# Performance work log

Measured on AMD Instinct MI355X. Metric: run time of the kernel, lower is better.

## Reference

```python
import jax, jax.numpy as jnp
import numpy as np

EMB = 1024

def setup_inputs() -> dict:
    key = jax.random.key(0)
    ks = jax.random.split(key, 6)
    B, S, E = 4, 2048, EMB
    x = jax.random.normal(ks[0], (B, S, E), dtype=jnp.float32)
    attention_mask = jax.random.randint(ks[1], (B, S, S), 0, 2, dtype=jnp.int32)
    proj_w = jax.random.normal(ks[2], (E, 3 * E), dtype=jnp.float32) * (1.0 / np.sqrt(E))
    proj_b = jax.random.normal(ks[3], (3 * E,), dtype=jnp.float32) * 0.02
    out_w = jax.random.normal(ks[4], (E, E), dtype=jnp.float32) * (1.0 / np.sqrt(E))
    out_b = jax.random.normal(ks[5], (E,), dtype=jnp.float32) * 0.02
    return {"x": x, "attention_mask": attention_mask, "proj_w": proj_w,
            "proj_b": proj_b, "out_w": out_w, "out_b": out_b}

def reference(x, attention_mask, proj_w, proj_b, out_w, out_b):
    E = x.shape[-1]
    scale = 1.0 / jnp.sqrt(jnp.asarray(E, x.dtype))
    qkv = x @ proj_w + proj_b                      # [B,S,3E]
    q, k, v = jnp.split(qkv, 3, axis=-1)           # each [B,S,E]
    scores = jnp.einsum('bqe,bke->bqk', q, k) * scale  # [B,S,S]
    scores = jnp.where(attention_mask == 0, jnp.asarray(-1e20, scores.dtype), scores)
    attn = jax.nn.softmax(scores, axis=-1)
    ctx = jnp.einsum('bqk,bke->bqe', attn, v)      # [B,S,E]
    return ctx @ out_w + out_b
```

## Files before the change

### kernel.cpp

```cpp
#include <hip/hip_runtime.h>
#include <cstdint>

typedef unsigned short u16;
typedef uint32_t u32;
typedef __bf16 bf16x8 __attribute__((ext_vector_type(8)));
typedef float f32x4 __attribute__((ext_vector_type(4)));

__device__ __forceinline__ u16 f2bf(float f) {
  unsigned u = __float_as_uint(f);
  u += 0x7fffu + ((u >> 16) & 1u);
  return (u16)(u >> 16);
}

__device__ __forceinline__ void async16(const void* g, void* l) {
  __builtin_amdgcn_global_load_lds(
      (const __attribute__((address_space(1))) uint32_t*)g,
      (__attribute__((address_space(3))) uint32_t*)l, 16, 0, 0);
}

__global__ __launch_bounds__(256) void k_prep(const float* __restrict__ x, u16* __restrict__ xb,
                                              const float* __restrict__ pw, u16* __restrict__ wt,
                                              const float* __restrict__ ow, u16* __restrict__ owt,
                                              const int* __restrict__ mask, u32* __restrict__ mbits) {
  const int bid = blockIdx.x;
  if (bid < 8192) {
    const int i = bid * 256 + threadIdx.x;
    const float4 v = ((const float4*)x)[i];
    ushort4 o;
    o.x = f2bf(v.x); o.y = f2bf(v.y); o.z = f2bf(v.z); o.w = f2bf(v.w);
    ((ushort4*)xb)[i] = o;
    return;
  }
  if (bid >= 12288) {
    const size_t w = (size_t)(bid - 12288) * 256 + threadIdx.x;
    const int* p = mask + w * 32;
    u32 bits = 0;
#pragma unroll
    for (int j = 0; j < 8; ++j) {
      const int4 v = ((const int4*)p)[j];
      bits |= (u32)(v.x & 1) << (j * 4 + 0);
      bits |= (u32)(v.y & 1) << (j * 4 + 1);
      bits |= (u32)(v.z & 1) << (j * 4 + 2);
      bits |= (u32)(v.w & 1) << (j * 4 + 3);
    }
    mbits[w] = bits;
    return;
  }
  __shared__ u16 tile[32][33];
  const int tx = threadIdx.x & 31, ty = threadIdx.x >> 5;
  const float* in;
  u16* outp;
  int lda, ldo, c0, r0;
  if (bid < 11264) {
    const int id = bid - 8192;
    c0 = (id % 96) * 32; r0 = (id / 96) * 32;
    in = pw; outp = wt; lda = 3072; ldo = 1024;
  } else {
    const int id = bid - 11264;
    c0 = (id % 32) * 32; r0 = (id / 32) * 32;
    in = ow; outp = owt; lda = 1024; ldo = 1024;
  }
#pragma unroll
  for (int i = 0; i < 4; ++i)
    tile[ty + i * 8][tx] = f2bf(in[(size_t)(r0 + ty + i * 8) * lda + c0 + tx]);
  __syncthreads();
#pragma unroll
  for (int i = 0; i < 4; ++i)
    outp[(size_t)(c0 + ty + i * 8) * ldo + r0 + tx] = tile[tx][ty + i * 8];
}

template <int MODE, int TM>
__global__ __launch_bounds__(256) void gemm_bt(
    const u16* __restrict__ A, long lda, long bsA,
    const u16* __restrict__ Bt, long ldb, long bsB,
    void* __restrict__ C, long ldc, long bsC,
    int M, int N, int K,
    const float* __restrict__ bias, const u32* __restrict__ mbits) {
  constexpr int MT = TM / 32;
  constexpr int ACALLS = TM / 8;
  constexpr int NC = (TM + 128) / 32;
  __shared__ u16 As[TM * 64];
  __shared__ u16 Bs[128 * 64];

  const int b = blockIdx.z;
  const int m0 = blockIdx.y * TM, n0 = blockIdx.x * 128;
  const int lane = threadIdx.x & 63;
  const int w = threadIdx.x >> 6;
  const int wr = w >> 1, wc = w & 1;

  const int srow = lane >> 3;
  const int scol = ((lane & 7) ^ ((lane >> 3) & 7)) * 8;
  const u16* pa = A + (size_t)b * bsA + (size_t)(m0 + srow) * lda + scol;
  const u16* pb = Bt + (size_t)b * bsB + (size_t)(n0 + srow) * ldb + scol;

  const int m_l = lane & 15, q = lane >> 4, m7 = m_l & 7;
  const int offs[2] = {(q ^ m7) * 8, ((4 + q) ^ m7) * 8};

  f32x4 acc[MT][4] = {};
  f32x4 accs[MT] = {};
  bf16x8 ones;
#pragma unroll
  for (int e = 0; e < 8; ++e) ones[e] = (__bf16)1.0f;

  for (int kt = 0; kt < K; kt += 64) {
    __syncthreads();
#pragma unroll
    for (int g = 0; g < NC; ++g) {
      const int idx = w * NC + g;
      if (idx < ACALLS)
        async16(pa + (size_t)(idx * 8) * lda, As + idx * 512);
      else
        async16(pb + (size_t)((idx - ACALLS) * 8) * ldb, Bs + (idx - ACALLS) * 512);
    }
    __syncthreads();
#pragma unroll
    for (int s = 0; s < 2; ++s) {
      bf16x8 af[MT], bfr[4];
#pragma unroll
      for (int t = 0; t < MT; ++t)
        af[t] = *(const bf16x8*)(As + (wr * (TM / 2) + t * 16 + m_l) * 64 + offs[s]);
#pragma unroll
      for (int t = 0; t < 4; ++t)
        bfr[t] = *(const bf16x8*)(Bs + (wc * 64 + t * 16 + m_l) * 64 + offs[s]);
#pragma unroll
      for (int mt = 0; mt < MT; ++mt)
#pragma unroll
        for (int nt = 0; nt < 4; ++nt)
          acc[mt][nt] = __builtin_amdgcn_mfma_f32_16x16x32_bf16(af[mt], bfr[nt], acc[mt][nt], 0, 0, 0);
      if constexpr (MODE == 2) {
#pragma unroll
        for (int mt = 0; mt < MT; ++mt)
          accs[mt] = __builtin_amdgcn_mfma_f32_16x16x32_bf16(af[mt], ones, accs[mt], 0, 0, 0);
      }
    }
    pa += 64;
    pb += 64;
  }

  if constexpr (MODE == 1) {
    __syncthreads();
    const int rl = threadIdx.x >> 1, pr = threadIdx.x & 1;
    const uint2 v = *(const uint2*)(mbits + ((size_t)(b * M + m0 + rl)) * (N >> 5) + (n0 >> 5) + pr * 2);
    ((u32*)As)[rl * 4 + pr * 2] = v.x;
    ((u32*)As)[rl * 4 + pr * 2 + 1] = v.y;
    __syncthreads();
  }

  float rinv[MT][4];
  if constexpr (MODE == 2) {
#pragma unroll
    for (int mt = 0; mt < MT; ++mt)
#pragma unroll
      for (int r = 0; r < 4; ++r) rinv[mt][r] = 1.0f / accs[mt][r];
  }

#pragma unroll
  for (int mt = 0; mt < MT; ++mt) {
#pragma unroll
    for (int nt = 0; nt < 4; ++nt) {
      const int col = n0 + wc * 64 + nt * 16 + m_l;
      const int row0 = m0 + wr * (TM / 2) + mt * 16 + q * 4;
      if constexpr (MODE == 3) {
        ushort4 o;
        o.x = f2bf(acc[mt][nt][0]); o.y = f2bf(acc[mt][nt][1]);
        o.z = f2bf(acc[mt][nt][2]); o.w = f2bf(acc[mt][nt][3]);
        *(ushort4*)((u16*)C + (size_t)b * bsC + (size_t)col * ldc + row0) = o;
      } else {
#pragma unroll
        for (int r = 0; r < 4; ++r) {
          const int row = row0 + r;
          float v = acc[mt][nt][r];
          if constexpr (MODE == 0) {
            v += bias[col];
            if (col < 1024) v *= 0.03125f;
            ((u16*)C)[(size_t)b * bsC + (size_t)row * ldc + col] = f2bf(v);
          } else if constexpr (MODE == 1) {
            const int cl = wc * 64 + nt * 16 + m_l;
            const int rl = wr * 64 + mt * 16 + q * 4 + r;
            const u32 wb = ((const u32*)As)[rl * 4 + (cl >> 5)];
            v = ((wb >> (cl & 31)) & 1u) ? __expf(fminf(v, 30.f)) : 0.f;
            ((u16*)C)[(size_t)b * bsC + (size_t)row * ldc + col] = f2bf(v);
          } else if constexpr (MODE == 2) {
            v = v * rinv[mt][r] + bias[col];
            ((float*)C)[(size_t)b * bsC + (size_t)row * ldc + col] = v;
          }
        }
      }
    }
  }
}

extern "C" void kernel_launch(void* const* d_in, const int* in_sizes, int n_in,
                              void* d_out, int out_size, void* d_ws, size_t ws_size,
                              hipStream_t stream) {
  const float* x = (const float*)d_in[0];
  const int* mask = (const int*)d_in[1];
  const float* proj_w = (const float*)d_in[2];
  const float* proj_b = (const float*)d_in[3];
  const float* out_w = (const float*)d_in[4];
  const float* out_b = (const float*)d_in[5];
  float* out = (float*)d_out;

  char* ws = (char*)d_ws;
  u16* xb = (u16*)(ws);
  u16* wt = (u16*)(ws + 16777216);
  u16* owt = (u16*)(ws + 23068672);
  u16* qkv = (u16*)(ws + 25165824);
  u16* P = (u16*)(ws + 75497472);
  u32* mbits = (u32*)(ws + 109051904);
  u16* Ut = (u16*)xb;

  k_prep<<<14336, 256, 0, stream>>>(x, xb, proj_w, wt, out_w, owt, mask, mbits);
  gemm_bt<0, 128><<<dim3(24, 64, 1), 256, 0, stream>>>(xb, 1024, 0, wt, 1024, 0, qkv, 3072, 0,
                                                       8192, 3072, 1024, proj_b, nullptr);
  gemm_bt<1, 128><<<dim3(16, 16, 4), 256, 0, stream>>>(
      qkv, 3072, (long)2048 * 3072, qkv + 1024, 3072, (long)2048 * 3072,
      P, 2048, (long)2048 * 2048, 2048, 2048, 1024, nullptr, mbits);
  gemm_bt<3, 64><<<dim3(8, 32, 4), 256, 0, stream>>>(
      qkv + 2048, 3072, (long)2048 * 3072, owt, 1024, 0,
      Ut, 2048, (long)1024 * 2048, 2048, 1024, 1024, nullptr, nullptr);
  gemm_bt<2, 64><<<dim3(8, 32, 4), 256, 0, stream>>>(
      P, 2048, (long)2048 * 2048, Ut, 2048, (long)1024 * 2048,
      out, 1024, (long)2048 * 1024, 2048, 1024, 2048, out_b, nullptr);
}
```

Baseline: 342.0 us.

## Merge scores and V-projection GEMMs into one launch, retile final GEMM

Folds the QK^T masked-exp GEMM and the V·Wout^T transpose GEMM, which are independent, into a single kernel that branches on blockIdx.z. The two run concurrently and one launch boundary goes away. The V-projection now uses 128x128 tiles (half the blocks in that z-range exit early). The final P·U GEMM moves to 64x64 tiles for twice as many blocks. The aim is better GPU fill and less launch/tail overhead, at the cost of idle blocks and smaller-tile efficiency in the last GEMM.

New measurement: 379.8 us. 1.11x slower.

```diff
diff --git a/kernel.cpp b/kernel.cpp
--- a/kernel.cpp
+++ b/kernel.cpp
@@ -69,21 +69,18 @@
     outp[(size_t)(c0 + ty + i * 8) * ldo + r0 + tx] = tile[tx][ty + i * 8];
 }
 
-template <int MODE, int TM>
-__global__ __launch_bounds__(256) void gemm_bt(
+template <int MODE, int TM, int BN>
+__device__ __forceinline__ void gemm_core(
+    u16* As, u16* Bs,
     const u16* __restrict__ A, long lda, long bsA,
     const u16* __restrict__ Bt, long ldb, long bsB,
     void* __restrict__ C, long ldc, long bsC,
     int M, int N, int K,
-    const float* __restrict__ bias, const u32* __restrict__ mbits) {
-  constexpr int MT = TM / 32;
-  constexpr int ACALLS = TM / 8;
-  constexpr int NC = (TM + 128) / 32;
-  __shared__ u16 As[TM * 64];
-  __shared__ u16 Bs[128 * 64];
-
-  const int b = blockIdx.z;
-  const int m0 = blockIdx.y * TM, n0 = blockIdx.x * 128;
+    const float* __restrict__ bias, const u32* __restrict__ mbits,
+    int b, int bx, int by) {
+  constexpr int MT = TM / 32, NT = BN / 32;
+  constexpr int ACALLS = TM / 8, TOT = (TM + BN) / 8, NC = TOT / 4;
+  const int m0 = by * TM, n0 = bx * BN;
   const int lane = threadIdx.x & 63;
   const int w = threadIdx.x >> 6;
   const int wr = w >> 1, wc = w & 1;
@@ -96,7 +93,7 @@
   const int m_l = lane & 15, q = lane >> 4, m7 = m_l & 7;
   const int offs[2] = {(q ^ m7) * 8, ((4 + q) ^ m7) * 8};
 
-  f32x4 acc[MT][4] = {};
+  f32x4 acc[MT][NT] = {};
   f32x4 accs[MT] = {};
   bf16x8 ones;
 #pragma unroll
@@ -115,17 +112,17 @@
     __syncthreads();
 #pragma unroll
     for (int s = 0; s < 2; ++s) {
-      bf16x8 af[MT], bfr[4];
+      bf16x8 af[MT], bfr[NT];
 #pragma unroll
       for (int t = 0; t < MT; ++t)
         af[t] = *(const bf16x8*)(As + (wr * (TM / 2) + t * 16 + m_l) * 64 + offs[s]);
 #pragma unroll
-      for (int t = 0; t < 4; ++t)
-        bfr[t] = *(const bf16x8*)(Bs + (wc * 64 + t * 16 + m_l) * 64 + offs[s]);
+      for (int t = 0; t < NT; ++t)
+        bfr[t] = *(const bf16x8*)(Bs + (wc * (BN / 2) + t * 16 + m_l) * 64 + offs[s]);
 #pragma unroll
       for (int mt = 0; mt < MT; ++mt)
 #pragma unroll
-        for (int nt = 0; nt < 4; ++nt)
+        for (int nt = 0; nt < NT; ++nt)
           acc[mt][nt] = __builtin_amdgcn_mfma_f32_16x16x32_bf16(af[mt], bfr[nt], acc[mt][nt], 0, 0, 0);
       if constexpr (MODE == 2) {
 #pragma unroll
@@ -157,8 +154,8 @@
 #pragma unroll
   for (int mt = 0; mt < MT; ++mt) {
 #pragma unroll
-    for (int nt = 0; nt < 4; ++nt) {
-      const int col = n0 + wc * 64 + nt * 16 + m_l;
+    for (int nt = 0; nt < NT; ++nt) {
+      const int col = n0 + wc * (BN / 2) + nt * 16 + m_l;
       const int row0 = m0 + wr * (TM / 2) + mt * 16 + q * 4;
       if constexpr (MODE == 3) {
         ushort4 o;
@@ -190,6 +187,39 @@
   }
 }
 
+template <int MODE, int TM, int BN>
+__global__ __launch_bounds__(256) void gemm_bt(
+    const u16* __restrict__ A, long lda, long bsA,
+    const u16* __restrict__ Bt, long ldb, long bsB,
+    void* __restrict__ C, long ldc, long bsC,
+    int M, int N, int K,
+    const float* __restrict__ bias, const u32* __restrict__ mbits) {
+  __shared__ u16 As[TM * 64];
+  __shared__ u16 Bs[BN * 64];
+  gemm_core<MODE, TM, BN>(As, Bs, A, lda, bsA, Bt, ldb, bsB, C, ldc, bsC, M, N, K,
+                          bias, mbits, blockIdx.z, blockIdx.x, blockIdx.y);
+}
+
+__global__ __launch_bounds__(256) void k_mid(
+    const u16* __restrict__ qkv, u16* __restrict__ P, u16* __restrict__ Ut,
+    const u16* __restrict__ owt, const u32* __restrict__ mbits) {
+  __shared__ u16 As[128 * 64];
+  __shared__ u16 Bs[128 * 64];
+  const int z = blockIdx.z;
+  if (z < 4) {
+    gemm_core<1, 128, 128>(As, Bs,
+        qkv, 3072, (long)2048 * 3072, qkv + 1024, 3072, (long)2048 * 3072,
+        P, 2048, (long)2048 * 2048, 2048, 2048, 1024, nullptr, mbits,
+        z, blockIdx.x, blockIdx.y);
+  } else {
+    if (blockIdx.x >= 8) return;
+    gemm_core<3, 128, 128>(As, Bs,
+        qkv + 2048, 3072, (long)2048 * 3072, owt, 1024, 0,
+        Ut, 2048, (long)1024 * 2048, 2048, 1024, 1024, nullptr, nullptr,
+        z - 4, blockIdx.x, blockIdx.y);
+  }
+}
+
 extern "C" void kernel_launch(void* const* d_in, const int* in_sizes, int n_in,
                               void* d_out, int out_size, void* d_ws, size_t ws_size,
                               hipStream_t stream) {
@@ -211,15 +241,10 @@
   u16* Ut = (u16*)xb;
 
   k_prep<<<14336, 256, 0, stream>>>(x, xb, proj_w, wt, out_w, owt, mask, mbits);
-  gemm_bt<0, 128><<<dim3(24, 64, 1), 256, 0, stream>>>(xb, 1024, 0, wt, 1024, 0, qkv, 3072, 0,
-                                                       8192, 3072, 1024, proj_b, nullptr);
-  gemm_bt<1, 128><<<dim3(16, 16, 4), 256, 0, stream>>>(
-      qkv, 3072, (long)2048 * 3072, qkv + 1024, 3072, (long)2048 * 3072,
-      P, 2048, (long)2048 * 2048, 2048, 2048, 1024, nullptr, mbits);
-  gemm_bt<3, 64><<<dim3(8, 32, 4), 256, 0, stream>>>(
-      qkv + 2048, 3072, (long)2048 * 3072, owt, 1024, 0,
-      Ut, 2048, (long)1024 * 2048, 2048, 1024, 1024, nullptr, nullptr);
-  gemm_bt<2, 64><<<dim3(8, 32, 4), 256, 0, stream>>>(
+  gemm_bt<0, 128, 128><<<dim3(24, 64, 1), 256, 0, stream>>>(
+      xb, 1024, 0, wt, 1024, 0, qkv, 3072, 0, 8192, 3072, 1024, proj_b, nullptr);
+  k_mid<<<dim3(16, 16, 8), 256, 0, stream>>>(qkv, P, Ut, owt, mbits);
+  gemm_bt<2, 64, 64><<<dim3(16, 32, 4), 256, 0, stream>>>(
       P, 2048, (long)2048 * 2048, Ut, 2048, (long)1024 * 2048,
       out, 1024, (long)2048 * 1024, 2048, 1024, 2048, out_b, nullptr);
 }
```
